# Performance work log

Measured on AMD Instinct MI355X. Metric: run time of the kernel, lower is better.

## Reference

```python
import jax, jax.numpy as jnp
import numpy as np

N_NODES = 50000
N_EDGES = 500000
D_IN = 128
HID = 128
OUT = 2
N_REL = 4
BN_EPS = 1e-5


def setup_inputs() -> dict:
    key = jax.random.key(0)
    ks = jax.random.split(key, 14)
    s_in = 1.0 / np.sqrt(D_IN)
    s_h = 1.0 / np.sqrt(HID)
    return {
        "x": jax.random.normal(ks[0], (N_NODES, D_IN), jnp.float32),
        "edge_index": jax.random.randint(ks[1], (N_REL, 2, N_EDGES), 0, N_NODES, jnp.int32),
        "W1": jax.random.normal(ks[2], (N_REL, D_IN, HID), jnp.float32) * s_in,
        "b1": jax.random.normal(ks[3], (N_REL, HID), jnp.float32) * s_in,
        "W2": jax.random.normal(ks[4], (N_REL, HID, HID), jnp.float32) * s_h,
        "b2": jax.random.normal(ks[5], (N_REL, HID), jnp.float32) * s_h,
        "bn_gamma": jnp.ones((HID,), jnp.float32),
        "bn_beta": jnp.zeros((HID,), jnp.float32),
        "lin1_W": jax.random.normal(ks[6], (HID, HID), jnp.float32) * s_h,
        "lin1_b": jax.random.normal(ks[7], (HID,), jnp.float32) * s_h,
        "lin2_W": jax.random.normal(ks[8], (HID, OUT), jnp.float32) * s_h,
        "lin2_b": jax.random.normal(ks[9], (OUT,), jnp.float32) * s_h,
    }


def _gcn(x, ei, W, b):
    # GCNConv: D^-1/2 (A + I) D^-1/2 (X W) + b
    n = x.shape[0]
    h = x @ W                                    # [N, H]
    loops = jnp.arange(n, dtype=ei.dtype)
    src = jnp.concatenate([ei[0], loops])        # add self loops
    dst = jnp.concatenate([ei[1], loops])
    deg = jax.ops.segment_sum(jnp.ones(dst.shape, h.dtype), dst, num_segments=n)
    dinv = jnp.where(deg > 0, jax.lax.rsqrt(deg), 0.0)
    norm = dinv[src] * dinv[dst]                 # [E+N]
    msg = h[src] * norm[:, None]                 # gather + scale
    return jax.ops.segment_sum(msg, dst, num_segments=n) + b


def _hetero(x, edge_index, W, b):
    # HeteroConv with aggr='sum' over the 4 relation types (same src/dst node type)
    out = _gcn(x, edge_index[0], W[0], b[0])
    for r in range(1, N_REL):
        out = out + _gcn(x, edge_index[r], W[r], b[r])
    return out


def reference(x, edge_index, W1, b1, W2, b2, bn_gamma, bn_beta, lin1_W, lin1_b, lin2_W, lin2_b):
    h = jax.nn.relu(_hetero(x, edge_index, W1, b1))
    h = jax.nn.relu(_hetero(h, edge_index, W2, b2))
    # BatchNorm1d (batch statistics, biased variance)
    mean = h.mean(axis=0)
    var = h.var(axis=0)
    h = (h - mean) * jax.lax.rsqrt(var + BN_EPS) * bn_gamma + bn_beta
    h = jax.nn.relu(h @ lin1_W + lin1_b)
    # dropout is identity in eval
    return h @ lin2_W + lin2_b
```

## Files before the change

kernel.cpp:

```cpp
#include <hip/hip_runtime.h>
#include <math.h>

#define NN 50000
#define NE 500000
#define NREL 4
#define D 128
#define RSZ 512
#define NRANGE 98
#define NBK (NREL * NRANGE)
#define BCAP 6144
#define NCH 128
#define CH 3907
#define FCAP 96
static constexpr float BN_EPS = 1e-5f;

typedef __attribute__((ext_vector_type(8))) short short8;
typedef __attribute__((ext_vector_type(4))) float f32x4;

__device__ __forceinline__ float bf2f(unsigned short u) {
    return __uint_as_float(((unsigned)u) << 16);
}
__device__ __forceinline__ unsigned short f2bf(float f) {
    unsigned x = __float_as_uint(f);
    return (unsigned short)((x + 0x7FFFu + ((x >> 16) & 1u)) >> 16);
}

__global__ __launch_bounds__(256) void k_zero(int* __restrict__ p, int n) {
    int i = blockIdx.x * blockDim.x + threadIdx.x;
    if (i < n) p[i] = 0;
}

__global__ __launch_bounds__(256) void k_bin(const int* __restrict__ ei,
                                             int* __restrict__ frag,
                                             int* __restrict__ cntg) {
    int c = blockIdx.x, r = blockIdx.y;
    const int* srcp = ei + r * 2 * NE;
    const int* dstp = srcp + NE;
    __shared__ int bins[NRANGE * FCAP];
    __shared__ int cnt[NRANGE];
    int tid = threadIdx.x;
    for (int i = tid; i < NRANGE; i += 256) cnt[i] = 0;
    __syncthreads();
    int e0 = c * CH, e1 = min(e0 + CH, NE);
    for (int e = e0 + tid; e < e1; e += 256) {
        int d = dstp[e];
        int s = srcp[e];
        int q = d >> 9;
        int pos = atomicAdd(&cnt[q], 1);
        if (pos < FCAP) bins[q * FCAP + pos] = s | ((d & 511) << 16);
    }
    __syncthreads();
    int w = tid >> 6, lane = tid & 63;
    for (int q = w; q < NRANGE; q += 4) {
        int k = min(cnt[q], FCAP);
        int gbase = ((r * NRANGE + q) * NCH + c) * FCAP;
        for (int i = lane; i < k; i += 64) frag[gbase + i] = bins[q * FCAP + i];
    }
    for (int q = tid; q < NRANGE; q += 256) cntg[(r * NRANGE + q) * NCH + c] = min(cnt[q], FCAP);
}

__global__ __launch_bounds__(512) void k_sortb(const int* __restrict__ frag,
                                               const int* __restrict__ cntg,
                                               unsigned short* __restrict__ csr,
                                               int* __restrict__ rstart,
                                               int* __restrict__ rend,
                                               float* __restrict__ dinv) {
    int q = blockIdx.x, r = blockIdx.y;
    int blk = r * NRANGE + q;
    int n0 = q * RSZ;
    int nrows = min(RSZ, NN - n0);
    __shared__ int cnts[NCH], cbase[NCH];
    __shared__ int stage[BCAP];
    __shared__ unsigned short csr_s[BCAP];
    __shared__ int hist[RSZ], off[RSZ], cnt2[RSZ];
    int tid = threadIdx.x;
    hist[tid] = 0;
    cnt2[tid] = 0;
    if (tid < NCH) cnts[tid] = cntg[blk * NCH + tid];
    __syncthreads();
    if (tid < NCH) cbase[tid] = cnts[tid];
    __syncthreads();
    for (int d = 1; d < NCH; d <<= 1) {
        int t = 0;
        if (tid < NCH && tid >= d) t = cbase[tid - d];
        __syncthreads();
        if (tid < NCH) cbase[tid] += t;
        __syncthreads();
    }
    if (tid < NCH) cbase[tid] -= cnts[tid];
    __syncthreads();
    int tot = cbase[NCH - 1] + cnts[NCH - 1];
    {
        int g = tid >> 2, l = tid & 3;
        int k = cnts[g], cb = cbase[g];
        int gbase = (blk * NCH + g) * FCAP;
        for (int i = l; i < k; i += 4)
            if (cb + i < BCAP) stage[cb + i] = frag[gbase + i];
    }
    __syncthreads();
    if (tot > BCAP) tot = BCAP;
    for (int i = tid; i < tot; i += 512) atomicAdd(&hist[(stage[i] >> 16) & 511], 1);
    __syncthreads();
    int h = hist[tid];
    if (tid < nrows) dinv[r * NN + n0 + tid] = rsqrtf((float)(h + 1));
    off[tid] = h;
    __syncthreads();
    for (int d = 1; d < RSZ; d <<= 1) {
        int t = (tid >= d) ? off[tid - d] : 0;
        __syncthreads();
        off[tid] += t;
        __syncthreads();
    }
    int excl = off[tid] - h;
    __syncthreads();
    off[tid] = excl;
    int base = blk * BCAP;
    if (tid < nrows) {
        rstart[r * NN + n0 + tid] = base + excl;
        rend[r * NN + n0 + tid] = base + excl + h;
    }
    __syncthreads();
    for (int i = tid; i < tot; i += 512) {
        int v = stage[i];
        int dl = (v >> 16) & 511;
        int p = atomicAdd(&cnt2[dl], 1);
        csr_s[off[dl] + p] = (unsigned short)(v & 0xFFFF);
    }
    __syncthreads();
    for (int i = tid; i < tot; i += 512) csr[base + i] = csr_s[i];
}

__global__ __launch_bounds__(256) void k_cast(const float* __restrict__ x, unsigned short* __restrict__ xb) {
    int i = blockIdx.x * 256 + threadIdx.x;
    if (i * 4 >= NN * D) return;
    float4 v = *(const float4*)(x + (size_t)i * 4);
    unsigned short u[4] = {f2bf(v.x), f2bf(v.y), f2bf(v.z), f2bf(v.w)};
    *(ushort4*)(xb + (size_t)i * 4) = *(ushort4*)u;
}

__global__ __launch_bounds__(256) void k_prep(const float* __restrict__ W1, const float* __restrict__ W2,
                                              const float* __restrict__ l1W, const float* __restrict__ b1,
                                              const float* __restrict__ b2, unsigned short* __restrict__ Wt1,
                                              unsigned short* __restrict__ Wt2, unsigned short* __restrict__ Wt3,
                                              float* __restrict__ bs1, float* __restrict__ bs2) {
    int blk = blockIdx.x, tid = threadIdx.x;
    if (blk < 256) {
        int i = blk * 256 + tid;
        int kk = i & 511, n = i >> 9;
        Wt1[n * 512 + kk] = f2bf(W1[kk * 128 + n]);
        Wt2[n * 512 + kk] = f2bf(W2[kk * 128 + n]);
    } else if (blk < 320) {
        int i = (blk - 256) * 256 + tid;
        int kk = i & 127, n = i >> 7;
        Wt3[n * 128 + kk] = f2bf(l1W[kk * 128 + n]);
    } else if (tid < 128) {
        bs1[tid] = b1[tid] + b1[128 + tid] + b1[256 + tid] + b1[384 + tid];
        bs2[tid] = b2[tid] + b2[128 + tid] + b2[256 + tid] + b2[384 + tid];
    }
}

__global__ __launch_bounds__(256) void k_agg(const unsigned short* __restrict__ in,
                                             const unsigned short* __restrict__ csr,
                                             const int* __restrict__ rstart,
                                             const int* __restrict__ rend,
                                             const float* __restrict__ dinv,
                                             unsigned short* __restrict__ Acat) {
    int r = blockIdx.y;
    int wave = threadIdx.x >> 6, lane = threadIdx.x & 63;
    int n = blockIdx.x * 4 + wave;
    if (n >= NN) return;
    const float* dv = dinv + r * NN;
    int start = rstart[r * NN + n], end = rend[r * NN + n];
    const ushort2* in2 = (const ushort2*)in;
    float ax = 0.f, ay = 0.f;
    int e = start;
    for (; e + 4 <= end; e += 4) {
        int s0 = csr[e], s1 = csr[e + 1], s2 = csr[e + 2], s3 = csr[e + 3];
        float w0 = dv[s0], w1 = dv[s1], w2 = dv[s2], w3 = dv[s3];
        ushort2 u0 = in2[s0 * 64 + lane];
        ushort2 u1 = in2[s1 * 64 + lane];
        ushort2 u2 = in2[s2 * 64 + lane];
        ushort2 u3 = in2[s3 * 64 + lane];
        ax = fmaf(bf2f(u0.x), w0, ax); ay = fmaf(bf2f(u0.y), w0, ay);
        ax = fmaf(bf2f(u1.x), w1, ax); ay = fmaf(bf2f(u1.y), w1, ay);
        ax = fmaf(bf2f(u2.x), w2, ax); ay = fmaf(bf2f(u2.y), w2, ay);
        ax = fmaf(bf2f(u3.x), w3, ax); ay = fmaf(bf2f(u3.y), w3, ay);
    }
    for (; e < end; e++) {
        int s = csr[e];
        float w = dv[s];
        ushort2 u = in2[s * 64 + lane];
        ax = fmaf(bf2f(u.x), w, ax);
        ay = fmaf(bf2f(u.y), w, ay);
    }
    float wn = dv[n];
    ushort2 us = in2[n * 64 + lane];
    ax = fmaf(bf2f(us.x), wn, ax);
    ay = fmaf(bf2f(us.y), wn, ay);
    ushort2 o;
    o.x = f2bf(wn * ax);
    o.y = f2bf(wn * ay);
    *(ushort2*)(Acat + (size_t)n * 512 + r * 128 + 2 * lane) = o;
}

template <int K, bool STATS>
__global__ __launch_bounds__(256) void k_mm(const unsigned short* __restrict__ A,
                                            const unsigned short* __restrict__ Bt,
                                            const float* __restrict__ bias,
                                            unsigned short* __restrict__ C,
                                            float* __restrict__ bnsum) {
    int tid = threadIdx.x;
    int w = tid >> 6, lane = tid & 63;
    int ln = lane & 15, quad = lane >> 4;
    int mwave = blockIdx.x * 256 + w * 64;

    f32x4 acc[4][8];
#pragma unroll
    for (int a = 0; a < 4; a++)
#pragma unroll
        for (int b = 0; b < 8; b++) acc[a][b] = (f32x4){0.f, 0.f, 0.f, 0.f};

    size_t arow[4];
#pragma unroll
    for (int mf = 0; mf < 4; mf++) {
        int m = mwave + mf * 16 + ln;
        arow[mf] = (size_t)min(m, NN - 1) * K;
    }
    size_t brow[8];
#pragma unroll
    for (int nf = 0; nf < 8; nf++) brow[nf] = (size_t)(nf * 16 + ln) * K;

    for (int k0 = 0; k0 < K; k0 += 32) {
        int kof = k0 + quad * 8;
        short8 af[4], bf[8];
#pragma unroll
        for (int mf = 0; mf < 4; mf++) af[mf] = *(const short8*)(A + arow[mf] + kof);
#pragma unroll
        for (int nf = 0; nf < 8; nf++) bf[nf] = *(const short8*)(Bt + brow[nf] + kof);
#pragma unroll
        for (int mf = 0; mf < 4; mf++)
#pragma unroll
            for (int nf = 0; nf < 8; nf++)
                acc[mf][nf] = __builtin_amdgcn_mfma_f32_16x16x32_bf16(af[mf], bf[nf], acc[mf][nf], 0, 0, 0);
    }

    float bs[8];
#pragma unroll
    for (int nf = 0; nf < 8; nf++) bs[nf] = bias[nf * 16 + ln];
    float sn[8], qn[8];
#pragma unroll
    for (int nf = 0; nf < 8; nf++) { sn[nf] = 0.f; qn[nf] = 0.f; }

#pragma unroll
    for (int mf = 0; mf < 4; mf++)
#pragma unroll
        for (int nf = 0; nf < 8; nf++)
#pragma unroll
            for (int rg = 0; rg < 4; rg++) {
                int m = mwave + mf * 16 + quad * 4 + rg;
                if (m < NN) {
                    float v = fmaxf(acc[mf][nf][rg] + bs[nf], 0.f);
                    if (STATS) { sn[nf] += v; qn[nf] += v * v; }
                    C[(size_t)m * 128 + nf * 16 + ln] = f2bf(v);
                }
            }

    if (STATS) {
#pragma unroll
        for (int nf = 0; nf < 8; nf++) {
            float s = sn[nf], q = qn[nf];
            s += __shfl_xor(s, 16); s += __shfl_xor(s, 32);
            q += __shfl_xor(q, 16); q += __shfl_xor(q, 32);
            if (quad == 0) {
                unsafeAtomicAdd(&bnsum[nf * 16 + ln], s);
                unsafeAtomicAdd(&bnsum[128 + nf * 16 + ln], q);
            }
        }
    }
}

__global__ __launch_bounds__(128) void k_bn_final(const float* __restrict__ sums,
                                                  const float* __restrict__ gamma,
                                                  const float* __restrict__ beta,
                                                  float* __restrict__ bnp) {
    int c = threadIdx.x;
    if (c < D) {
        float mean = sums[c] / (float)NN;
        float var = sums[D + c] / (float)NN - mean * mean;
        float sc = gamma[c] * rsqrtf(var + BN_EPS);
        bnp[c] = sc;
        bnp[D + c] = beta[c] - mean * sc;
    }
}

__global__ __launch_bounds__(256) void k_final(const unsigned short* __restrict__ R2,
                                               const float* __restrict__ bnp,
                                               const unsigned short* __restrict__ Wt3,
                                               const float* __restrict__ l1b,
                                               const float* __restrict__ l2W,
                                               const float* __restrict__ l2b,
                                               float* __restrict__ out) {
    int tid = threadIdx.x;
    int w = tid >> 6, lane = tid & 63;
    int ln = lane & 15, quad = lane >> 4;
    int mwave = blockIdx.x * 256 + w * 64;

    f32x4 acc[4][8];
#pragma unroll
    for (int a = 0; a < 4; a++)
#pragma unroll
        for (int b = 0; b < 8; b++) acc[a][b] = (f32x4){0.f, 0.f, 0.f, 0.f};

    size_t arow[4];
#pragma unroll
    for (int mf = 0; mf < 4; mf++) {
        int m = mwave + mf * 16 + ln;
        arow[mf] = (size_t)min(m, NN - 1) * 128;
    }
    size_t brow[8];
#pragma unroll
    for (int nf = 0; nf < 8; nf++) brow[nf] = (size_t)(nf * 16 + ln) * 128;

    for (int k0 = 0; k0 < 128; k0 += 32) {
        int kof = k0 + quad * 8;
        float4 scA = *(const float4*)(bnp + kof);
        float4 scB = *(const float4*)(bnp + kof + 4);
        float4 shA = *(const float4*)(bnp + 128 + kof);
        float4 shB = *(const float4*)(bnp + 128 + kof + 4);
        float scv[8] = {scA.x, scA.y, scA.z, scA.w, scB.x, scB.y, scB.z, scB.w};
        float shv[8] = {shA.x, shA.y, shA.z, shA.w, shB.x, shB.y, shB.z, shB.w};
        short8 af[4], bf[8];
#pragma unroll
        for (int mf = 0; mf < 4; mf++) {
            short8 rv = *(const short8*)(R2 + arow[mf] + kof);
            unsigned short ab[8];
#pragma unroll
            for (int j = 0; j < 8; j++)
                ab[j] = f2bf(bf2f((unsigned short)rv[j]) * scv[j] + shv[j]);
            af[mf] = *(short8*)ab;
        }
#pragma unroll
        for (int nf = 0; nf < 8; nf++) bf[nf] = *(const short8*)(Wt3 + brow[nf] + kof);
#pragma unroll
        for (int mf = 0; mf < 4; mf++)
#pragma unroll
            for (int nf = 0; nf < 8; nf++)
                acc[mf][nf] = __builtin_amdgcn_mfma_f32_16x16x32_bf16(af[mf], bf[nf], acc[mf][nf], 0, 0, 0);
    }

    float b1v[8], w0[8], w1[8];
#pragma unroll
    for (int nf = 0; nf < 8; nf++) {
        int n = nf * 16 + ln;
        b1v[nf] = l1b[n];
        w0[nf] = l2W[n * 2];
        w1[nf] = l2W[n * 2 + 1];
    }
    float ob0 = l2b[0], ob1 = l2b[1];
#pragma unroll
    for (int mf = 0; mf < 4; mf++)
#pragma unroll
        for (int rg = 0; rg < 4; rg++) {
            float p0 = 0.f, p1 = 0.f;
#pragma unroll
            for (int nf = 0; nf < 8; nf++) {
                float y = fmaxf(acc[mf][nf][rg] + b1v[nf], 0.f);
                p0 += y * w0[nf];
                p1 += y * w1[nf];
            }
            p0 += __shfl_xor(p0, 1); p0 += __shfl_xor(p0, 2);
            p0 += __shfl_xor(p0, 4); p0 += __shfl_xor(p0, 8);
            p1 += __shfl_xor(p1, 1); p1 += __shfl_xor(p1, 2);
            p1 += __shfl_xor(p1, 4); p1 += __shfl_xor(p1, 8);
            int m = mwave + mf * 16 + quad * 4 + rg;
            if (ln == 0 && m < NN) {
                out[(size_t)m * 2 + 0] = p0 + ob0;
                out[(size_t)m * 2 + 1] = p1 + ob1;
            }
        }
}

extern "C" void kernel_launch(void* const* d_in, const int* in_sizes, int n_in,
                              void* d_out, int out_size, void* d_ws, size_t ws_size,
                              hipStream_t stream) {
    const float* x = (const float*)d_in[0];
    const int* ei = (const int*)d_in[1];
    const float* W1 = (const float*)d_in[2];
    const float* b1 = (const float*)d_in[3];
    const float* W2 = (const float*)d_in[4];
    const float* b2 = (const float*)d_in[5];
    const float* gamma = (const float*)d_in[6];
    const float* beta = (const float*)d_in[7];
    const float* l1W = (const float*)d_in[8];
    const float* l1b = (const float*)d_in[9];
    const float* l2W = (const float*)d_in[10];
    const float* l2b = (const float*)d_in[11];
    float* out = (float*)d_out;

    char* ws = (char*)d_ws;
    size_t off = 0;
    auto alloc = [&](size_t bytes) {
        void* p = ws + off;
        off += (bytes + 255) & ~(size_t)255;
        return p;
    };
    float* dinv = (float*)alloc((size_t)NREL * NN * sizeof(float));
    int* rstart = (int*)alloc((size_t)NREL * NN * sizeof(int));
    int* rend = (int*)alloc((size_t)NREL * NN * sizeof(int));
    unsigned short* csr = (unsigned short*)alloc((size_t)NBK * BCAP * 2);
    unsigned short* xb = (unsigned short*)alloc((size_t)NN * D * 2);
    unsigned short* Acat = (unsigned short*)alloc((size_t)NN * 512 * 2);
    unsigned short* h1b = (unsigned short*)alloc((size_t)NN * D * 2);
    unsigned short* R2b = (unsigned short*)alloc((size_t)NN * D * 2);
    unsigned short* Wt1 = (unsigned short*)alloc(128 * 512 * 2);
    unsigned short* Wt2 = (unsigned short*)alloc(128 * 512 * 2);
    unsigned short* Wt3 = (unsigned short*)alloc(128 * 128 * 2);
    float* bs1 = (float*)alloc(128 * sizeof(float));
    float* bs2 = (float*)alloc(128 * sizeof(float));
    float* bnsum = (float*)alloc(256 * sizeof(float));
    float* bnp = (float*)alloc(256 * sizeof(float));

    int* frag = (int*)Acat;
    int* cntg = frag + (size_t)NREL * NRANGE * NCH * FCAP;

    k_zero<<<1, 256, 0, stream>>>((int*)bnsum, 256);
    k_prep<<<321, 256, 0, stream>>>(W1, W2, l1W, b1, b2, Wt1, Wt2, Wt3, bs1, bs2);
    k_cast<<<(NN * D / 4 + 255) / 256, 256, 0, stream>>>(x, xb);
    dim3 bgrid(NCH, NREL);
    k_bin<<<bgrid, 256, 0, stream>>>(ei, frag, cntg);
    dim3 sgrid(NRANGE, NREL);
    k_sortb<<<sgrid, 512, 0, stream>>>(frag, cntg, csr, rstart, rend, dinv);

    dim3 agrid((NN + 3) / 4, NREL);
    k_agg<<<agrid, 256, 0, stream>>>(xb, csr, rstart, rend, dinv, Acat);
    k_mm<512, false><<<(NN + 255) / 256, 256, 0, stream>>>(Acat, Wt1, bs1, h1b, nullptr);
    k_agg<<<agrid, 256, 0, stream>>>(h1b, csr, rstart, rend, dinv, Acat);
    k_mm<512, true><<<(NN + 255) / 256, 256, 0, stream>>>(Acat, Wt2, bs2, R2b, bnsum);
    k_bn_final<<<1, 128, 0, stream>>>(bnsum, gamma, beta, bnp);
    k_final<<<(NN + 255) / 256, 256, 0, stream>>>(R2b, bnp, Wt3, l1b, l2W, l2b, out);
}
```

Before: 445.1 us.

## Merge prep kernels and aggregate all four relations per wave

Merges the zero, weight-prep and cast kernels into one launch to cut launch overhead. Rewrites the aggregation kernel so each wave handles one node across all four relations at once, interleaving the four edge lists in a single loop. The self-loop feature row is loaded once instead of four times, and there are four independent gathers in flight per iteration. The cost is predicated idle lanes when relation degrees differ and higher register use.

```diff
diff --git a/kernel.cpp b/kernel.cpp
--- a/kernel.cpp
+++ b/kernel.cpp
@@ -12,6 +12,7 @@
 #define NCH 128
 #define CH 3907
 #define FCAP 96
+#define CAST_BLKS 6250
 static constexpr float BN_EPS = 1e-5f;
 
 typedef __attribute__((ext_vector_type(8))) short short8;
@@ -25,9 +26,38 @@
     return (unsigned short)((x + 0x7FFFu + ((x >> 16) & 1u)) >> 16);
 }
 
-__global__ __launch_bounds__(256) void k_zero(int* __restrict__ p, int n) {
-    int i = blockIdx.x * blockDim.x + threadIdx.x;
-    if (i < n) p[i] = 0;
+__global__ __launch_bounds__(256) void k_pre(const float* __restrict__ x,
+                                             const float* __restrict__ W1, const float* __restrict__ W2,
+                                             const float* __restrict__ l1W, const float* __restrict__ b1,
+                                             const float* __restrict__ b2,
+                                             unsigned short* __restrict__ xb,
+                                             unsigned short* __restrict__ Wt1,
+                                             unsigned short* __restrict__ Wt2,
+                                             unsigned short* __restrict__ Wt3,
+                                             float* __restrict__ bs1, float* __restrict__ bs2,
+                                             float* __restrict__ bnsum) {
+    int blk = blockIdx.x, tid = threadIdx.x;
+    if (blk < CAST_BLKS) {
+        int i = blk * 256 + tid;
+        float4 v = *(const float4*)(x + (size_t)i * 4);
+        unsigned short u[4] = {f2bf(v.x), f2bf(v.y), f2bf(v.z), f2bf(v.w)};
+        *(ushort4*)(xb + (size_t)i * 4) = *(ushort4*)u;
+    } else if (blk < CAST_BLKS + 256) {
+        int i = (blk - CAST_BLKS) * 256 + tid;
+        int kk = i & 511, n = i >> 9;
+        Wt1[n * 512 + kk] = f2bf(W1[kk * 128 + n]);
+        Wt2[n * 512 + kk] = f2bf(W2[kk * 128 + n]);
+    } else if (blk < CAST_BLKS + 320) {
+        int i = (blk - CAST_BLKS - 256) * 256 + tid;
+        int kk = i & 127, n = i >> 7;
+        Wt3[n * 128 + kk] = f2bf(l1W[kk * 128 + n]);
+    } else {
+        if (tid < 128) {
+            bs1[tid] = b1[tid] + b1[128 + tid] + b1[256 + tid] + b1[384 + tid];
+            bs2[tid] = b2[tid] + b2[128 + tid] + b2[256 + tid] + b2[384 + tid];
+        }
+        bnsum[tid] = 0.f;
+    }
 }
 
 __global__ __launch_bounds__(256) void k_bin(const int* __restrict__ ei,
@@ -130,77 +160,59 @@
     for (int i = tid; i < tot; i += 512) csr[base + i] = csr_s[i];
 }
 
-__global__ __launch_bounds__(256) void k_cast(const float* __restrict__ x, unsigned short* __restrict__ xb) {
-    int i = blockIdx.x * 256 + threadIdx.x;
-    if (i * 4 >= NN * D) return;
-    float4 v = *(const float4*)(x + (size_t)i * 4);
-    unsigned short u[4] = {f2bf(v.x), f2bf(v.y), f2bf(v.z), f2bf(v.w)};
-    *(ushort4*)(xb + (size_t)i * 4) = *(ushort4*)u;
-}
-
-__global__ __launch_bounds__(256) void k_prep(const float* __restrict__ W1, const float* __restrict__ W2,
-                                              const float* __restrict__ l1W, const float* __restrict__ b1,
-                                              const float* __restrict__ b2, unsigned short* __restrict__ Wt1,
-                                              unsigned short* __restrict__ Wt2, unsigned short* __restrict__ Wt3,
-                                              float* __restrict__ bs1, float* __restrict__ bs2) {
-    int blk = blockIdx.x, tid = threadIdx.x;
-    if (blk < 256) {
-        int i = blk * 256 + tid;
-        int kk = i & 511, n = i >> 9;
-        Wt1[n * 512 + kk] = f2bf(W1[kk * 128 + n]);
-        Wt2[n * 512 + kk] = f2bf(W2[kk * 128 + n]);
-    } else if (blk < 320) {
-        int i = (blk - 256) * 256 + tid;
-        int kk = i & 127, n = i >> 7;
-        Wt3[n * 128 + kk] = f2bf(l1W[kk * 128 + n]);
-    } else if (tid < 128) {
-        bs1[tid] = b1[tid] + b1[128 + tid] + b1[256 + tid] + b1[384 + tid];
-        bs2[tid] = b2[tid] + b2[128 + tid] + b2[256 + tid] + b2[384 + tid];
-    }
-}
-
 __global__ __launch_bounds__(256) void k_agg(const unsigned short* __restrict__ in,
                                              const unsigned short* __restrict__ csr,
                                              const int* __restrict__ rstart,
                                              const int* __restrict__ rend,
                                              const float* __restrict__ dinv,
                                              unsigned short* __restrict__ Acat) {
-    int r = blockIdx.y;
     int wave = threadIdx.x >> 6, lane = threadIdx.x & 63;
     int n = blockIdx.x * 4 + wave;
     if (n >= NN) return;
-    const float* dv = dinv + r * NN;
-    int start = rstart[r * NN + n], end = rend[r * NN + n];
     const ushort2* in2 = (const ushort2*)in;
-    float ax = 0.f, ay = 0.f;
-    int e = start;
-    for (; e + 4 <= end; e += 4) {
-        int s0 = csr[e], s1 = csr[e + 1], s2 = csr[e + 2], s3 = csr[e + 3];
-        float w0 = dv[s0], w1 = dv[s1], w2 = dv[s2], w3 = dv[s3];
+    int e0 = rstart[0 * NN + n], E0 = rend[0 * NN + n];
+    int e1 = rstart[1 * NN + n], E1 = rend[1 * NN + n];
+    int e2 = rstart[2 * NN + n], E2 = rend[2 * NN + n];
+    int e3 = rstart[3 * NN + n], E3 = rend[3 * NN + n];
+    int L0 = max(E0 - 1, 0), L1 = max(E1 - 1, 0);
+    int L2 = max(E2 - 1, 0), L3 = max(E3 - 1, 0);
+    float ax0 = 0.f, ay0 = 0.f, ax1 = 0.f, ay1 = 0.f;
+    float ax2 = 0.f, ay2 = 0.f, ax3 = 0.f, ay3 = 0.f;
+    while ((e0 < E0) | (e1 < E1) | (e2 < E2) | (e3 < E3)) {
+        bool a0 = e0 < E0, a1 = e1 < E1, a2 = e2 < E2, a3 = e3 < E3;
+        int i0 = a0 ? e0 : L0;
+        int i1 = a1 ? e1 : L1;
+        int i2 = a2 ? e2 : L2;
+        int i3 = a3 ? e3 : L3;
+        int s0 = csr[i0], s1 = csr[i1], s2 = csr[i2], s3 = csr[i3];
+        float w0 = a0 ? dinv[0 * NN + s0] : 0.f;
+        float w1 = a1 ? dinv[1 * NN + s1] : 0.f;
+        float w2 = a2 ? dinv[2 * NN + s2] : 0.f;
+        float w3 = a3 ? dinv[3 * NN + s3] : 0.f;
         ushort2 u0 = in2[s0 * 64 + lane];
         ushort2 u1 = in2[s1 * 64 + lane];
         ushort2 u2 = in2[s2 * 64 + lane];
         ushort2 u3 = in2[s3 * 64 + lane];
-        ax = fmaf(bf2f(u0.x), w0, ax); ay = fmaf(bf2f(u0.y), w0, ay);
-        ax = fmaf(bf2f(u1.x), w1, ax); ay = fmaf(bf2f(u1.y), w1, ay);
-        ax = fmaf(bf2f(u2.x), w2, ax); ay = fmaf(bf2f(u2.y), w2, ay);
-        ax = fmaf(bf2f(u3.x), w3, ax); ay = fmaf(bf2f(u3.y), w3, ay);
-    }
-    for (; e < end; e++) {
-        int s = csr[e];
-        float w = dv[s];
-        ushort2 u = in2[s * 64 + lane];
-        ax = fmaf(bf2f(u.x), w, ax);
-        ay = fmaf(bf2f(u.y), w, ay);
-    }
-    float wn = dv[n];
+        ax0 = fmaf(bf2f(u0.x), w0, ax0); ay0 = fmaf(bf2f(u0.y), w0, ay0);
+        ax1 = fmaf(bf2f(u1.x), w1, ax1); ay1 = fmaf(bf2f(u1.y), w1, ay1);
+        ax2 = fmaf(bf2f(u2.x), w2, ax2); ay2 = fmaf(bf2f(u2.y), w2, ay2);
+        ax3 = fmaf(bf2f(u3.x), w3, ax3); ay3 = fmaf(bf2f(u3.y), w3, ay3);
+        e0 += a0; e1 += a1; e2 += a2; e3 += a3;
+    }
     ushort2 us = in2[n * 64 + lane];
-    ax = fmaf(bf2f(us.x), wn, ax);
-    ay = fmaf(bf2f(us.y), wn, ay);
+    float sx = bf2f(us.x), sy = bf2f(us.y);
+    float wn0 = dinv[0 * NN + n], wn1 = dinv[1 * NN + n];
+    float wn2 = dinv[2 * NN + n], wn3 = dinv[3 * NN + n];
+    unsigned short* orow = Acat + (size_t)n * 512 + 2 * lane;
     ushort2 o;
-    o.x = f2bf(wn * ax);
-    o.y = f2bf(wn * ay);
-    *(ushort2*)(Acat + (size_t)n * 512 + r * 128 + 2 * lane) = o;
+    o.x = f2bf(wn0 * fmaf(sx, wn0, ax0)); o.y = f2bf(wn0 * fmaf(sy, wn0, ay0));
+    *(ushort2*)(orow + 0) = o;
+    o.x = f2bf(wn1 * fmaf(sx, wn1, ax1)); o.y = f2bf(wn1 * fmaf(sy, wn1, ay1));
+    *(ushort2*)(orow + 128) = o;
+    o.x = f2bf(wn2 * fmaf(sx, wn2, ax2)); o.y = f2bf(wn2 * fmaf(sy, wn2, ay2));
+    *(ushort2*)(orow + 256) = o;
+    o.x = f2bf(wn3 * fmaf(sx, wn3, ax3)); o.y = f2bf(wn3 * fmaf(sy, wn3, ay3));
+    *(ushort2*)(orow + 384) = o;
 }
 
 template <int K, bool STATS>
@@ -423,15 +435,14 @@
     int* frag = (int*)Acat;
     int* cntg = frag + (size_t)NREL * NRANGE * NCH * FCAP;
 
-    k_zero<<<1, 256, 0, stream>>>((int*)bnsum, 256);
-    k_prep<<<321, 256, 0, stream>>>(W1, W2, l1W, b1, b2, Wt1, Wt2, Wt3, bs1, bs2);
-    k_cast<<<(NN * D / 4 + 255) / 256, 256, 0, stream>>>(x, xb);
+    k_pre<<<CAST_BLKS + 321, 256, 0, stream>>>(x, W1, W2, l1W, b1, b2, xb, Wt1, Wt2, Wt3,
+                                               bs1, bs2, bnsum);
     dim3 bgrid(NCH, NREL);
     k_bin<<<bgrid, 256, 0, stream>>>(ei, frag, cntg);
     dim3 sgrid(NRANGE, NREL);
     k_sortb<<<sgrid, 512, 0, stream>>>(frag, cntg, csr, rstart, rend, dinv);
 
-    dim3 agrid((NN + 3) / 4, NREL);
+    int agrid = (NN + 3) / 4;
     k_agg<<<agrid, 256, 0, stream>>>(xb, csr, rstart, rend, dinv, Acat);
     k_mm<512, false><<<(NN + 255) / 256, 256, 0, stream>>>(Acat, Wt1, bs1, h1b, nullptr);
     k_agg<<<agrid, 256, 0, stream>>>(h1b, csr, rstart, rend, dinv, Acat);
```

Measured after the change: 499.7 us. +12.3%, slower.
